# Kernel optimization log

Measured on AMD Instinct MI355X. Metric: run time of the kernel, lower is better.

## Reference

```python
import jax, jax.numpy as jnp
import numpy as np

L_LAYERS = 2
SEQ = 2048
K_EIG = 24
D = 128
D_TGT = 64
K_U = 3
K_Y = 2
B = 8


def hankel_eigh(n, k):
    # Z[i,j] = 2 / ((i+j)^3 - (i+j)), 1-indexed; top-k eigenpairs
    s = np.arange(1, n + 1, dtype=np.float64)
    ij = s[:, None] + s[None, :]
    z = 2.0 / (ij ** 3 - ij)
    vals, vecs = np.linalg.eigh(z)
    return (jnp.asarray(vals[-k:], jnp.float32), jnp.asarray(vecs[:, -k:], jnp.float32))


def setup_inputs() -> dict:
    key = jax.random.key(0)
    ks = jax.random.split(key, 8)
    sd = 1.0 / np.sqrt(D)
    inp = {
        "x": jax.random.normal(ks[0], (B, SEQ, D), jnp.float32),
        "emb_w": jax.random.normal(ks[1], (D, D), jnp.float32) * sd,
        "emb_b": jnp.zeros((D,), jnp.float32),
        "ln_g": jnp.ones((L_LAYERS, D), jnp.float32),
        "ln_b": jnp.zeros((L_LAYERS, D), jnp.float32),
        "m_phi": jax.random.normal(ks[2], (L_LAYERS, K_EIG * D, D), jnp.float32) * sd,
        "m_u": jax.random.normal(ks[3], (L_LAYERS, D, D, K_U), jnp.float32) * sd,
        "m_y": jax.random.normal(ks[4], (L_LAYERS, D, K_Y, D), jnp.float32) * 0.01,
        "w1": jax.random.normal(ks[5], (L_LAYERS, D, 2 * D), jnp.float32) * sd,
        "b1": jnp.zeros((L_LAYERS, 2 * D), jnp.float32),
        "proj_w": jax.random.normal(ks[6], (D, D_TGT), jnp.float32) * sd,
        "proj_b": jnp.zeros((D_TGT,), jnp.float32),
    }
    ev, evec = hankel_eigh(SEQ, K_EIG)
    inp["eig_vals"] = ev
    inp["eig_vecs"] = evec
    return inp


def compute_x_tilde(x, eig_vals, eig_vecs):
    # x: [B, L, D]; causal (truncated full) convolution of each eigvec filter
    # with each input channel via FFT. Result [B, L, K, D] -> [B, L, K*D].
    n = 2 * SEQ
    V = jnp.fft.rfft(eig_vecs, n=n, axis=0)              # [nf, K]
    U = jnp.fft.rfft(x, n=n, axis=1)                     # [B, nf, D]
    conv = jnp.fft.irfft(V[None, :, :, None] * U[:, :, None, :], n=n, axis=1)[:, :SEQ]
    conv = conv * (eig_vals ** 0.25)[None, None, :, None]
    return conv.reshape(x.shape[0], SEQ, K_EIG * x.shape[-1]).astype(x.dtype)


def compute_ar_x_preds(m_u, x):
    # o[t] = sum_{i<K_U} m_u[:, :, i] @ x[t-i]  (zero for t-i < 0)
    res = jnp.einsum('bli,oi->blo', x, m_u[:, :, 0])
    for i in range(1, K_U):
        xi = jnp.pad(x, ((0, 0), (i, 0), (0, 0)))[:, :SEQ]
        res = res + jnp.einsum('bli,oi->blo', xi, m_u[:, :, i])
    return res


def compute_y_t(m_y, deltas):
    # y[t] = sum_{j<K_Y} m_y[:, j, :] @ y[t-1-j] + deltas[t]
    d = deltas.shape[-1]
    def step(carry, x):  # carry [B, K_Y, d] holds y[t-1], y[t-2], ...
        out = jnp.einsum('okd,bkd->bo', m_y, carry) + x
        carry = jnp.concatenate([out[:, None, :], carry[:, :-1]], axis=1)
        return carry, out
    init = jnp.zeros((deltas.shape[0], K_Y, d), deltas.dtype)
    _, ys = jax.lax.scan(step, init, jnp.swapaxes(deltas, 0, 1))
    return jnp.swapaxes(ys, 0, 1)


def layer_norm(x, g, b):
    mu = x.mean(-1, keepdims=True)
    var = ((x - mu) ** 2).mean(-1, keepdims=True)
    return (x - mu) / jnp.sqrt(var + 1e-5) * g + b


def reference(x, emb_w, emb_b, ln_g, ln_b, m_phi, m_u, m_y, w1, b1, proj_w, proj_b, eig_vals, eig_vecs):
    h = x @ emb_w + emb_b
    for i in range(L_LAYERS):
        z = h
        h = layer_norm(h, ln_g[i], ln_b[i])
        x_tilde = compute_x_tilde(h, eig_vals, eig_vecs)       # [B, L, K*D]
        delta = x_tilde @ m_phi[i] + compute_ar_x_preds(m_u[i], h)
        y = compute_y_t(m_y[i], delta)
        y = jax.nn.gelu(y, approximate=False)
        y = y @ w1[i] + b1[i]
        a, g = jnp.split(y, 2, axis=-1)
        h = a * jax.nn.sigmoid(g) + z                          # GLU + residual (dropout=0)
    return h @ proj_w + proj_b
```

## Files before the change

### kernel.cpp

```cpp
#include <hip/hip_runtime.h>

typedef unsigned short u16;
typedef unsigned int u32;
typedef __bf16 bf16x8 __attribute__((ext_vector_type(8)));
typedef float f32x4 __attribute__((ext_vector_type(4)));
typedef float f32x2 __attribute__((ext_vector_type(2)));
typedef u16 u16x4 __attribute__((ext_vector_type(4)));
typedef u16 u16x8 __attribute__((ext_vector_type(8)));

#define DEV static __device__ __forceinline__

static constexpr int ROWS = 8 * 2048;
static constexpr int TAPS = 24;
static constexpr int PADR = 64;
static constexpr int DROWS = 2048 + PADR;

DEV u16 f2bf(float x) {
  u32 u = __float_as_uint(x);
  u += 0x7fffu + ((u >> 16) & 1u);
  return (u16)(u >> 16);
}

DEV void gld_lds16(const u16* g, u16* l) {
  __builtin_amdgcn_global_load_lds(
      (const __attribute__((address_space(1))) u32*)g,
      (__attribute__((address_space(3))) u32*)l, 16, 0, 0);
}


__global__ void prep_toeplitz(const float* __restrict__ evec,
                              const float* __restrict__ evals,
                              u16* __restrict__ T) {
  int k = blockIdx.x / 33, ti = blockIdx.x % 33;
  float sc = powf(evals[k], 0.25f);
  u16* out = T + (size_t)blockIdx.x * 4096;
  for (int e = threadIdx.x; e < 4096; e += 256) {
    int i = e >> 6, j = e & 63;
    int tau = (ti - 1) * 64 + i - j;
    float v = (tau >= 0 && tau < 2048) ? evec[tau * 24 + k] * sc : 0.f;
    out[e] = f2bf(v);
  }
}

__global__ __launch_bounds__(128) void hprep_kernel(const float* __restrict__ my,
                                                    u16* __restrict__ Hp) {
  const int l = blockIdx.x >> 7, j = blockIdx.x & 127;
  const int o = threadIdx.x;
  const float* M = my + (size_t)l * 32768;
  u32 mp1[64], mp2[64];
  {
    const float* r1 = M + (size_t)o * 256;
    const float* r2 = r1 + 128;
#pragma unroll
    for (int q = 0; q < 64; ++q) {
      mp1[q] = (u32)f2bf(r1[2 * q]) | ((u32)f2bf(r1[2 * q + 1]) << 16);
      mp2[q] = (u32)f2bf(r2[2 * q]) | ((u32)f2bf(r2[2 * q + 1]) << 16);
    }
  }
  __shared__ float vb[3][128];
  u16* HpL = Hp + ((size_t)l * 128 + o) * (TAPS * 128) + j;
  float v0 = (o == j) ? 1.f : 0.f;
  vb[0][o] = v0;
  vb[2][o] = 0.f;
  HpL[0] = f2bf(v0);
  __syncthreads();
  for (int tau = 1; tau < TAPS; ++tau) {
    const int a = (tau + 2) % 3;
    const int b = (tau + 1) % 3;
    const int c = tau % 3;
    const float* v1 = vb[a];
    const float* v2 = vb[b];
    float acc = 0.f;
#pragma unroll
    for (int q = 0; q < 64; ++q) {
      u32 w1 = mp1[q], w2 = mp2[q];
      float m1lo = __uint_as_float(w1 << 16);
      float m1hi = __uint_as_float(w1 & 0xffff0000u);
      float m2lo = __uint_as_float(w2 << 16);
      float m2hi = __uint_as_float(w2 & 0xffff0000u);
      acc += m1lo * v1[2 * q] + m1hi * v1[2 * q + 1];
      acc += m2lo * v2[2 * q] + m2hi * v2[2 * q + 1];
    }
    vb[c][o] = acc;
    HpL[tau * 128] = f2bf(acc);
    __syncthreads();
  }
}

__global__ __launch_bounds__(256) void prep_misc(
    const float* __restrict__ emb_w, const float* __restrict__ w1,
    const float* __restrict__ proj_w, const float* __restrict__ mphi,
    const float* __restrict__ mu, const float* __restrict__ x,
    u16* __restrict__ embT, u16* __restrict__ w1T, u16* __restrict__ projT,
    u16* __restrict__ mphiT, u16* __restrict__ xbf, u16* __restrict__ dpad,
    u16* __restrict__ xtc) {
  const int blk = blockIdx.x, tid = threadIdx.x;
  if (blk < 64) {
    int idx = blk * 256 + tid;
    int n = idx >> 7, k = idx & 127;
    embT[idx] = f2bf(emb_w[k * 128 + n]);
  } else if (blk < 320) {
    int l = (blk - 64) >> 7;
    int idx = ((blk - 64) & 127) * 256 + tid;
    int n = idx >> 7, k = idx & 127;
    w1T[l * 32768 + idx] = f2bf(w1[l * 32768 + k * 256 + n]);
  } else if (blk < 352) {
    int idx = (blk - 320) * 256 + tid;
    int n = idx >> 7, k = idx & 127;
    projT[idx] = f2bf(proj_w[k * 64 + n]);
  } else if (blk < 3808) {
    int l = (blk - 352) / 1728;
    int idx = ((blk - 352) % 1728) * 256 + tid;
    int o = idx / 3456, c = idx % 3456;
    float v;
    if (c < 3072) {
      v = mphi[(size_t)l * 3072 * 128 + (size_t)c * 128 + o];
    } else {
      int cc = c - 3072;
      int j = cc >> 7, i = cc & 127;
      v = mu[(size_t)l * 128 * 128 * 3 + ((size_t)o * 128 + i) * 3 + j];
    }
    mphiT[(size_t)l * 128 * 3456 + idx] = f2bf(v);
  } else if (blk < 5856) {
    int i = (blk - 3808) * 256 + tid;
    f32x4 v = *(const f32x4*)(x + (size_t)i * 4);
    u16x4 o;
    o[0] = f2bf(v[0]); o[1] = f2bf(v[1]); o[2] = f2bf(v[2]); o[3] = f2bf(v[3]);
    *(u16x4*)(xbf + (size_t)i * 4) = o;
  } else if (blk < 5888) {
    int i = (blk - 5856) * 256 + tid;
    int b = i >> 10, off = i & 1023;
    *(u16x8*)(dpad + (size_t)b * DROWS * 128 + off * 8) =
        (u16x8){0, 0, 0, 0, 0, 0, 0, 0};
  } else {
    for (int e = tid; e < 3072; e += 256) {
      int b = e / 384, r = e % 384;
      size_t addr;
      if (r < 256) addr = ((size_t)b * 2048 + 0) * 3456 + 3200 + r;
      else addr = ((size_t)b * 2048 + 1) * 3456 + 3328 + (r - 256);
      xtc[addr] = 0;
    }
  }
}


__global__ __launch_bounds__(256) void ln_tr_kernel(
    const float* __restrict__ h, const float* __restrict__ gam,
    const float* __restrict__ bet, u16* __restrict__ hlnT,
    u16* __restrict__ xtc) {
  __shared__ u16 tile[64][136];
  const int b = blockIdx.x >> 5, st = blockIdx.x & 31;
  const int wrow = threadIdx.x >> 6;
  const int lane = threadIdx.x & 63;
  f32x2 g2 = *(const f32x2*)(gam + lane * 2);
  f32x2 b2 = *(const f32x2*)(bet + lane * 2);
#pragma unroll 4
  for (int it = 0; it < 16; ++it) {
    int lr = it * 4 + wrow;
    int t = st * 64 + lr;
    size_t row = (size_t)b * 2048 + t;
    f32x2 v = *(const f32x2*)(h + row * 128 + lane * 2);
    float s = v[0] + v[1];
#pragma unroll
    for (int o = 32; o; o >>= 1) s += __shfl_xor(s, o);
    float mu = s * (1.f / 128.f);
    float dx = v[0] - mu, dy = v[1] - mu;
    float q = dx * dx + dy * dy;
#pragma unroll
    for (int o = 32; o; o >>= 1) q += __shfl_xor(q, o);
    float rstd = rsqrtf(q * (1.f / 128.f) + 1e-5f);
    float o0 = dx * rstd * g2[0] + b2[0];
    float o1 = dy * rstd * g2[1] + b2[1];
    u32 pk = (u32)f2bf(o0) | ((u32)f2bf(o1) << 16);
    *(u32*)&tile[lr][lane * 2] = pk;
    *(u32*)&xtc[row * 3456 + 3072 + lane * 2] = pk;
    if (t + 1 < 2048) *(u32*)&xtc[(row + 1) * 3456 + 3200 + lane * 2] = pk;
    if (t + 2 < 2048) *(u32*)&xtc[(row + 2) * 3456 + 3328 + lane * 2] = pk;
  }
  __syncthreads();
  const int d = threadIdx.x >> 1;
  const int half = threadIdx.x & 1;
#pragma unroll
  for (int i = 0; i < 4; ++i) {
    int sg = half * 4 + i;
    u16x8 w;
#pragma unroll
    for (int j = 0; j < 8; ++j) w[j] = tile[sg * 8 + j][d];
    *(u16x8*)(hlnT + ((size_t)b * 128 + d) * 2048 + st * 64 + sg * 8) = w;
  }
}


template <int BM, int BN, int WROWS, int WCOLS>
__global__ __launch_bounds__(256) void gemm_bt(
    const u16* __restrict__ A, int lda, const u16* __restrict__ BT, int ldbt,
    float* __restrict__ C, int ldc, const float* __restrict__ bias, int kBlocks) {
  constexpr int WTM = BM / WROWS;
  constexpr int WTN = BN / WCOLS;
  constexpr int FM = WTM / 16;
  constexpr int FN = WTN / 16;
  static_assert(FM >= 1 && FN >= 1, "tile too small");
  __shared__ u16 As[BM * 64];
  __shared__ u16 Bs[BN * 64];
  const int tid = threadIdx.x;
  const int wid = tid >> 6, lane = tid & 63;
  const int bm = blockIdx.x, bn = blockIdx.y;
  const int wr = wid / WCOLS, wc = wid % WCOLS;
  const int r = lane & 15, hi = lane >> 4;

  f32x4 acc[FM][FN];
#pragma unroll
  for (int i = 0; i < FM; ++i)
#pragma unroll
    for (int j = 0; j < FN; ++j) acc[i][j] = (f32x4){0.f, 0.f, 0.f, 0.f};

  for (int kb = 0; kb < kBlocks; ++kb) {
    if (kb) __syncthreads();
#pragma unroll
    for (int it = 0; it < BM / 32; ++it) {
      int ci = it * 256 + tid;
      int sc = (ci & 7) ^ ((ci >> 3) & 7);
      gld_lds16(A + (size_t)(bm * BM + (ci >> 3)) * lda + kb * 64 + sc * 8,
                &As[(it * 256 + wid * 64) * 8]);
    }
#pragma unroll
    for (int it = 0; it < BN / 32; ++it) {
      int ci = it * 256 + tid;
      int sc = (ci & 7) ^ ((ci >> 3) & 7);
      gld_lds16(BT + (size_t)(bn * BN + (ci >> 3)) * ldbt + kb * 64 + sc * 8,
                &Bs[(it * 256 + wid * 64) * 8]);
    }
    __syncthreads();
#pragma unroll
    for (int ks = 0; ks < 2; ++ks) {
      const int sk = ((ks * 4 + hi) ^ (r & 7)) << 3;
      bf16x8 af[FM], bfv[FN];
#pragma unroll
      for (int fm = 0; fm < FM; ++fm)
        af[fm] = *(const bf16x8*)&As[(wr * WTM + fm * 16 + r) * 64 + sk];
#pragma unroll
      for (int fn = 0; fn < FN; ++fn)
        bfv[fn] = *(const bf16x8*)&Bs[(wc * WTN + fn * 16 + r) * 64 + sk];
#pragma unroll
      for (int fm = 0; fm < FM; ++fm)
#pragma unroll
        for (int fn = 0; fn < FN; ++fn)
          acc[fm][fn] = __builtin_amdgcn_mfma_f32_16x16x32_bf16(
              af[fm], bfv[fn], acc[fm][fn], 0, 0, 0);
    }
  }
#pragma unroll
  for (int fm = 0; fm < FM; ++fm) {
#pragma unroll
    for (int fn = 0; fn < FN; ++fn) {
      const int col = bn * BN + wc * WTN + fn * 16 + r;
      const float bv = bias ? bias[col] : 0.f;
#pragma unroll
      for (int q = 0; q < 4; ++q) {
        const int row = bm * BM + wr * WTM + fm * 16 + hi * 4 + q;
        C[(size_t)row * ldc + col] = acc[fm][fn][q] + bv;
      }
    }
  }
}

__global__ __launch_bounds__(256) void gemm_delta(
    const u16* __restrict__ A, const u16* __restrict__ BT,
    u16* __restrict__ dpad) {
  __shared__ u16 As[2][32 * 64];
  __shared__ u16 Bs[2][128 * 64];
  const int tid = threadIdx.x;
  const int wid = tid >> 6, lane = tid & 63;
  const int bm = blockIdx.x;
  const int wr = wid >> 1, wc = wid & 1;
  const int r = lane & 15, hi = lane >> 4;

  f32x4 acc[4];
#pragma unroll
  for (int j = 0; j < 4; ++j) acc[j] = (f32x4){0.f, 0.f, 0.f, 0.f};

  auto stage = [&](int kb, int p) {
    {
      int ci = tid;
      int sc = (ci & 7) ^ ((ci >> 3) & 7);
      gld_lds16(A + (size_t)(bm * 32 + (ci >> 3)) * 3456 + kb * 64 + sc * 8,
                &As[p][(wid * 64) * 8]);
    }
#pragma unroll
    for (int it = 0; it < 4; ++it) {
      int ci = it * 256 + tid;
      int sc = (ci & 7) ^ ((ci >> 3) & 7);
      gld_lds16(BT + (size_t)(ci >> 3) * 3456 + kb * 64 + sc * 8,
                &Bs[p][(it * 256 + wid * 64) * 8]);
    }
  };

  stage(0, 0);
  __syncthreads();
  for (int kb = 0; kb < 54; ++kb) {
    const int p = kb & 1;
    if (kb < 53) stage(kb + 1, p ^ 1);
#pragma unroll
    for (int ks = 0; ks < 2; ++ks) {
      const int sk = ((ks * 4 + hi) ^ (r & 7)) << 3;
      bf16x8 af = *(const bf16x8*)&As[p][(wr * 16 + r) * 64 + sk];
      bf16x8 bfv[4];
#pragma unroll
      for (int fn = 0; fn < 4; ++fn)
        bfv[fn] = *(const bf16x8*)&Bs[p][(wc * 64 + fn * 16 + r) * 64 + sk];
#pragma unroll
      for (int fn = 0; fn < 4; ++fn)
        acc[fn] = __builtin_amdgcn_mfma_f32_16x16x32_bf16(af, bfv[fn], acc[fn], 0, 0, 0);
    }
    __syncthreads();
  }
#pragma unroll
  for (int fn = 0; fn < 4; ++fn) {
    const int col = wc * 64 + fn * 16 + r;
#pragma unroll
    for (int q = 0; q < 4; ++q) {
      const int row = bm * 32 + wr * 16 + hi * 4 + q;
      int bb = row >> 11, t = row & 2047;
      dpad[((size_t)(bb * DROWS + PADR + t)) * 128 + col] = f2bf(acc[fn][q]);
    }
  }
}

__global__ __launch_bounds__(256) void gemm_conv(
    const u16* __restrict__ T, const u16* __restrict__ hlnT,
    u16* __restrict__ xtc) {
  __shared__ u16 As[2][64 * 64];
  __shared__ u16 Bs[128 * 64];
  const int tid = threadIdx.x;
  const int wid = tid >> 6, lane = tid & 63;
  const int tt = blockIdx.x / 192;
  const int rem = blockIdx.x % 192;
  const int kc = rem >> 3, b = rem & 7;
  const int t0 = (15 - tt) << 7;
  const int r = lane & 15, hi = lane >> 4;
  const int wr = wid >> 1, wc = wid & 1;

  f32x4 acc[4][4];
#pragma unroll
  for (int i = 0; i < 4; ++i)
#pragma unroll
    for (int j = 0; j < 4; ++j) acc[i][j] = (f32x4){0.f, 0.f, 0.f, 0.f};

  const u16* Tk = T + (size_t)kc * 33 * 4096;
  const u16* Bb = hlnT + (size_t)b * 128 * 2048;
  const int base = t0 >> 6;
  const int nsb = base + 2;

  for (int sb = 0; sb < nsb; ++sb) {
    const int dlt = base - sb;
    const int p = sb & 1;
    if (sb) __syncthreads();
#pragma unroll
    for (int it = 0; it < 2; ++it) {
      int ci = it * 256 + tid;
      int sc = (ci & 7) ^ ((ci >> 3) & 7);
      gld_lds16(Tk + (size_t)(dlt + 1) * 4096 + (ci >> 3) * 64 + sc * 8,
                &As[p][(it * 256 + wid * 64) * 8]);
    }
    if (sb == 0) {
#pragma unroll
      for (int it = 0; it < 2; ++it) {
        int ci = it * 256 + tid;
        int sc = (ci & 7) ^ ((ci >> 3) & 7);
        gld_lds16(Tk + (size_t)(dlt + 2) * 4096 + (ci >> 3) * 64 + sc * 8,
                  &As[1][(it * 256 + wid * 64) * 8]);
      }
    }
#pragma unroll
    for (int it = 0; it < 4; ++it) {
      int ci = it * 256 + tid;
      int sc = (ci & 7) ^ ((ci >> 3) & 7);
      gld_lds16(Bb + (size_t)(ci >> 3) * 2048 + sb * 64 + sc * 8,
                &Bs[(it * 256 + wid * 64) * 8]);
    }
    __syncthreads();
    const u16* Aw = As[p ^ wr];
#pragma unroll
    for (int ks = 0; ks < 2; ++ks) {
      const int sk = ((ks * 4 + hi) ^ (r & 7)) << 3;
      bf16x8 af[4], bfv[4];
#pragma unroll
      for (int fm = 0; fm < 4; ++fm)
        af[fm] = *(const bf16x8*)&Aw[(fm * 16 + r) * 64 + sk];
#pragma unroll
      for (int fn = 0; fn < 4; ++fn)
        bfv[fn] = *(const bf16x8*)&Bs[(wc * 64 + fn * 16 + r) * 64 + sk];
#pragma unroll
      for (int fm = 0; fm < 4; ++fm)
#pragma unroll
        for (int fn = 0; fn < 4; ++fn)
          acc[fm][fn] = __builtin_amdgcn_mfma_f32_16x16x32_bf16(
              af[fm], bfv[fn], acc[fm][fn], 0, 0, 0);
    }
  }
#pragma unroll
  for (int fm = 0; fm < 4; ++fm) {
#pragma unroll
    for (int fn = 0; fn < 4; ++fn) {
      const int col = wc * 64 + fn * 16 + r;
#pragma unroll
      for (int q = 0; q < 4; ++q) {
        const int row = t0 + wr * 64 + fm * 16 + hi * 4 + q;
        xtc[((size_t)(b * 2048 + row)) * 3456 + kc * 128 + col] = f2bf(acc[fm][fn][q]);
      }
    }
  }
}

__global__ __launch_bounds__(256) void gemm_yconv(
    const u16* __restrict__ dpad, const u16* __restrict__ Hp,
    u16* __restrict__ ybf) {
  __shared__ u16 As[64 * 128];
  __shared__ u16 Bs[64 * 128];
  const int tid = threadIdx.x;
  const int wid = tid >> 6, lane = tid & 63;
  const int bm = blockIdx.x, bn = blockIdx.y;
  const int b = bm >> 5, t0 = (bm & 31) << 6;
  const int r = lane & 15, hi = lane >> 4;

  f32x4 acc[4];
#pragma unroll
  for (int j = 0; j < 4; ++j) acc[j] = (f32x4){0.f, 0.f, 0.f, 0.f};

  const u16* Ab = dpad + (size_t)b * DROWS * 128;
  for (int tap = 0; tap < TAPS; ++tap) {
    const u16* Ap = Ab + (size_t)(PADR + t0 - tap) * 128;
    if (tap) __syncthreads();
#pragma unroll
    for (int it = 0; it < 4; ++it) {
      int ci = it * 256 + tid;
      int row = ci >> 4;
      int sc = (ci & 15) ^ (row & 7);
      gld_lds16(Ap + (size_t)row * 128 + sc * 8,
                &As[(it * 256 + wid * 64) * 8]);
    }
#pragma unroll
    for (int it = 0; it < 4; ++it) {
      int ci = it * 256 + tid;
      int row = ci >> 4;
      int sc = (ci & 15) ^ (row & 7);
      gld_lds16(Hp + (size_t)(bn * 64 + row) * (TAPS * 128) + tap * 128 + sc * 8,
                &Bs[(it * 256 + wid * 64) * 8]);
    }
    __syncthreads();
#pragma unroll
    for (int ks = 0; ks < 4; ++ks) {
      const int sk = ((ks * 4 + hi) ^ (r & 7)) << 3;
      bf16x8 af = *(const bf16x8*)&As[(wid * 16 + r) * 128 + sk];
      bf16x8 bfv[4];
#pragma unroll
      for (int fn = 0; fn < 4; ++fn)
        bfv[fn] = *(const bf16x8*)&Bs[(fn * 16 + r) * 128 + sk];
#pragma unroll
      for (int fn = 0; fn < 4; ++fn)
        acc[fn] = __builtin_amdgcn_mfma_f32_16x16x32_bf16(af, bfv[fn], acc[fn], 0, 0, 0);
    }
  }
#pragma unroll
  for (int fn = 0; fn < 4; ++fn) {
    const int col = bn * 64 + fn * 16 + r;
#pragma unroll
    for (int q = 0; q < 4; ++q) {
      const int row = t0 + wid * 16 + hi * 4 + q;
      float v = acc[fn][q];
      float gl = 0.5f * v * (1.f + erff(v * 0.70710678118654752f));
      ybf[((size_t)(b * 2048 + row)) * 128 + col] = f2bf(gl);
    }
  }
}

__global__ __launch_bounds__(256) void gemm_w1glu(
    const u16* __restrict__ ybf, const u16* __restrict__ w1T,
    const float* __restrict__ b1, float* __restrict__ h,
    u16* __restrict__ hbf) {
  __shared__ u16 As[32 * 64];
  __shared__ u16 Bs[256 * 64];
  __shared__ float sg[32][128];
  const int tid = threadIdx.x;
  const int wid = tid >> 6, lane = tid & 63;
  const int bm = blockIdx.x;
  const int wr = wid >> 1, wc = wid & 1;
  const int r = lane & 15, hi = lane >> 4;

  f32x4 acc[8];
#pragma unroll
  for (int j = 0; j < 8; ++j) acc[j] = (f32x4){0.f, 0.f, 0.f, 0.f};

  for (int kb = 0; kb < 2; ++kb) {
    if (kb) __syncthreads();
    {
      int ci = tid;
      int sc = (ci & 7) ^ ((ci >> 3) & 7);
      gld_lds16(ybf + (size_t)(bm * 32 + (ci >> 3)) * 128 + kb * 64 + sc * 8,
                &As[(wid * 64) * 8]);
    }
#pragma unroll
    for (int it = 0; it < 8; ++it) {
      int ci = it * 256 + tid;
      int sc = (ci & 7) ^ ((ci >> 3) & 7);
      gld_lds16(w1T + (size_t)(ci >> 3) * 128 + kb * 64 + sc * 8,
                &Bs[(it * 256 + wid * 64) * 8]);
    }
    __syncthreads();
#pragma unroll
    for (int ks = 0; ks < 2; ++ks) {
      const int sk = ((ks * 4 + hi) ^ (r & 7)) << 3;
      bf16x8 af = *(const bf16x8*)&As[(wr * 16 + r) * 64 + sk];
      bf16x8 bfv[8];
#pragma unroll
      for (int fn = 0; fn < 8; ++fn)
        bfv[fn] = *(const bf16x8*)&Bs[(wc * 128 + fn * 16 + r) * 64 + sk];
#pragma unroll
      for (int fn = 0; fn < 8; ++fn)
        acc[fn] = __builtin_amdgcn_mfma_f32_16x16x32_bf16(af, bfv[fn], acc[fn], 0, 0, 0);
    }
  }
  __syncthreads();
  if (wc == 1) {
#pragma unroll
    for (int fn = 0; fn < 8; ++fn) {
      const int colg = fn * 16 + r;
      const float bv = b1[128 + colg];
#pragma unroll
      for (int q = 0; q < 4; ++q) {
        const int rl = wr * 16 + hi * 4 + q;
        float v = acc[fn][q] + bv;
        sg[rl][colg] = 1.f / (1.f + expf(-v));
      }
    }
  }
  __syncthreads();
  if (wc == 0) {
#pragma unroll
    for (int fn = 0; fn < 8; ++fn) {
      const int col = fn * 16 + r;
      const float bv = b1[col];
#pragma unroll
      for (int q = 0; q < 4; ++q) {
        const int rl = wr * 16 + hi * 4 + q;
        const size_t row = (size_t)bm * 32 + rl;
        float a = acc[fn][q] + bv;
        float hn = a * sg[rl][col] + h[row * 128 + col];
        h[row * 128 + col] = hn;
        hbf[row * 128 + col] = f2bf(hn);
      }
    }
  }
}


extern "C" void kernel_launch(void* const* d_in, const int* in_sizes, int n_in,
                              void* d_out, int out_size, void* d_ws, size_t ws_size,
                              hipStream_t stream) {
  (void)in_sizes; (void)n_in; (void)out_size; (void)ws_size;
  const float* x = (const float*)d_in[0];
  const float* emb_w = (const float*)d_in[1];
  const float* emb_b = (const float*)d_in[2];
  const float* ln_g = (const float*)d_in[3];
  const float* ln_b = (const float*)d_in[4];
  const float* m_phi = (const float*)d_in[5];
  const float* m_u = (const float*)d_in[6];
  const float* m_y = (const float*)d_in[7];
  const float* w1 = (const float*)d_in[8];
  const float* b1 = (const float*)d_in[9];
  const float* proj_w = (const float*)d_in[10];
  const float* proj_b = (const float*)d_in[11];
  const float* evals = (const float*)d_in[12];
  const float* evec = (const float*)d_in[13];
  float* out = (float*)d_out;

  char* p = (char*)d_ws;
  auto carve = [&](size_t bytes) {
    char* r = p;
    p += (bytes + 255) & ~(size_t)255;
    return r;
  };
  u16* Tbuf = (u16*)carve((size_t)24 * 33 * 4096 * 2);
  u16* embT = (u16*)carve(128 * 128 * 2);
  u16* w1T = (u16*)carve((size_t)2 * 256 * 128 * 2);
  u16* projT = (u16*)carve(64 * 128 * 2);
  u16* mphiT = (u16*)carve((size_t)2 * 128 * 3456 * 2);
  u16* Hp = (u16*)carve((size_t)2 * 128 * TAPS * 128 * 2);
  u16* xbf = (u16*)carve((size_t)ROWS * 128 * 2);
  float* h = (float*)carve((size_t)ROWS * 128 * 4);
  u16* hbf = (u16*)carve((size_t)ROWS * 128 * 2);
  u16* hlnT = (u16*)carve((size_t)ROWS * 128 * 2);
  u16* xtc = (u16*)carve((size_t)ROWS * 3456 * 2);
  u16* dpad = (u16*)carve((size_t)8 * DROWS * 128 * 2);
  u16* ybf = (u16*)carve((size_t)ROWS * 128 * 2);

  prep_toeplitz<<<dim3(24 * 33), dim3(256), 0, stream>>>(evec, evals, Tbuf);
  hprep_kernel<<<dim3(256), dim3(128), 0, stream>>>(m_y, Hp);
  prep_misc<<<dim3(5889), dim3(256), 0, stream>>>(
      emb_w, w1, proj_w, m_phi, m_u, x, embT, w1T, projT, mphiT, xbf, dpad, xtc);

  gemm_bt<32, 128, 2, 2><<<dim3(512, 1), dim3(256), 0, stream>>>(
      xbf, 128, embT, 128, h, 128, emb_b, 2);

  for (int l = 0; l < 2; ++l) {
    const u16* mT = mphiT + (size_t)l * 128 * 3456;
    ln_tr_kernel<<<dim3(256), dim3(256), 0, stream>>>(
        h, ln_g + l * 128, ln_b + l * 128, hlnT, xtc);
    gemm_conv<<<dim3(3072), dim3(256), 0, stream>>>(Tbuf, hlnT, xtc);
    gemm_delta<<<dim3(512), dim3(256), 0, stream>>>(xtc, mT, dpad);
    gemm_yconv<<<dim3(256, 2), dim3(256), 0, stream>>>(
        dpad, Hp + (size_t)l * 128 * TAPS * 128, ybf);
    gemm_w1glu<<<dim3(512), dim3(256), 0, stream>>>(
        ybf, w1T + (size_t)l * 256 * 128, b1 + l * 256, h, hbf);
  }

  gemm_bt<32, 64, 2, 2><<<dim3(512, 1), dim3(256), 0, stream>>>(
      hbf, 128, projT, 128, out, 64, proj_b, 2);
}
```

Baseline: 465.6 us.

## Double gemm_conv output tile to 256 rows with 512 threads sharing B tiles

The Toeplitz convolution GEMM now covers 256 time steps per block using 8 waves instead of 128 steps with 4 waves. It keeps a 4-slot ring of Toeplitz A tiles so each B (hln) tile loaded into LDS feeds four row groups rather than two, and it halves the grid. This cuts redundant global loads of the hln tiles, but fewer and larger blocks may reduce occupancy and worsen causal load imbalance across blocks.

New measurement: 540.7 us. 1.16x slower.

```diff
diff --git a/kernel.cpp b/kernel.cpp
--- a/kernel.cpp
+++ b/kernel.cpp
@@ -326,17 +326,18 @@
   }
 }
 
-__global__ __launch_bounds__(256) void gemm_conv(
+__global__ __launch_bounds__(512) void gemm_conv(
     const u16* __restrict__ T, const u16* __restrict__ hlnT,
     u16* __restrict__ xtc) {
-  __shared__ u16 As[2][64 * 64];
+  __shared__ u16 As[4][64 * 64];
   __shared__ u16 Bs[128 * 64];
   const int tid = threadIdx.x;
   const int wid = tid >> 6, lane = tid & 63;
   const int tt = blockIdx.x / 192;
   const int rem = blockIdx.x % 192;
   const int kc = rem >> 3, b = rem & 7;
-  const int t0 = (15 - tt) << 7;
+  const int t0 = (7 - tt) << 8;
+  const int base4 = t0 >> 6;
   const int r = lane & 15, hi = lane >> 4;
   const int wr = wid >> 1, wc = wid & 1;
 
@@ -348,38 +349,38 @@
 
   const u16* Tk = T + (size_t)kc * 33 * 4096;
   const u16* Bb = hlnT + (size_t)b * 128 * 2048;
-  const int base = t0 >> 6;
-  const int nsb = base + 2;
-
-  for (int sb = 0; sb < nsb; ++sb) {
-    const int dlt = base - sb;
-    const int p = sb & 1;
-    if (sb) __syncthreads();
+  const int nsb = base4 + 4;
+
+  auto stageA = [&](int v) {
+    int ti = v < 0 ? 0 : v;
+    int sc = (tid & 7) ^ ((tid >> 3) & 7);
+    gld_lds16(Tk + (size_t)ti * 4096 + (tid >> 3) * 64 + sc * 8,
+              &As[v & 3][(wid * 64) * 8]);
+  };
+  auto stageB = [&](int sb) {
 #pragma unroll
     for (int it = 0; it < 2; ++it) {
-      int ci = it * 256 + tid;
-      int sc = (ci & 7) ^ ((ci >> 3) & 7);
-      gld_lds16(Tk + (size_t)(dlt + 1) * 4096 + (ci >> 3) * 64 + sc * 8,
-                &As[p][(it * 256 + wid * 64) * 8]);
-    }
-    if (sb == 0) {
-#pragma unroll
-      for (int it = 0; it < 2; ++it) {
-        int ci = it * 256 + tid;
-        int sc = (ci & 7) ^ ((ci >> 3) & 7);
-        gld_lds16(Tk + (size_t)(dlt + 2) * 4096 + (ci >> 3) * 64 + sc * 8,
-                  &As[1][(it * 256 + wid * 64) * 8]);
-      }
-    }
-#pragma unroll
-    for (int it = 0; it < 4; ++it) {
-      int ci = it * 256 + tid;
+      int ci = it * 512 + tid;
       int sc = (ci & 7) ^ ((ci >> 3) & 7);
       gld_lds16(Bb + (size_t)(ci >> 3) * 2048 + sb * 64 + sc * 8,
-                &Bs[(it * 256 + wid * 64) * 8]);
-    }
+                &Bs[(it * 512 + wid * 64) * 8]);
+    }
+  };
+
+  for (int sb = 0; sb < nsb; ++sb) {
+    const int vbase = base4 - sb + 1;
+    if (sb) {
+      __syncthreads();
+      stageA(vbase);
+    } else {
+      stageA(vbase);
+      stageA(vbase + 1);
+      stageA(vbase + 2);
+      stageA(vbase + 3);
+    }
+    stageB(sb);
     __syncthreads();
-    const u16* Aw = As[p ^ wr];
+    const u16* Aw = As[(vbase + wr) & 3];
 #pragma unroll
     for (int ks = 0; ks < 2; ++ks) {
       const int sk = ((ks * 4 + hi) ^ (r & 7)) << 3;
@@ -606,7 +607,7 @@
     const u16* mT = mphiT + (size_t)l * 128 * 3456;
     ln_tr_kernel<<<dim3(256), dim3(256), 0, stream>>>(
         h, ln_g + l * 128, ln_b + l * 128, hlnT, xtc);
-    gemm_conv<<<dim3(3072), dim3(256), 0, stream>>>(Tbuf, hlnT, xtc);
+    gemm_conv<<<dim3(1536), dim3(512), 0, stream>>>(Tbuf, hlnT, xtc);
     gemm_delta<<<dim3(512), dim3(256), 0, stream>>>(xtc, mT, dpad);
     gemm_yconv<<<dim3(256, 2), dim3(256), 0, stream>>>(
         dpad, Hp + (size_t)l * 128 * TAPS * 128, ybf);
```
